# Kernel tuning notes

Measured on AMD Instinct MI355X. Metric: run time of the kernel, lower is better.

Reference implementation:

```python
import jax, jax.numpy as jnp
import numpy as np

N, E = 50000, 800000
HID, HEADS, EDIM = 64, 4, 3
NEG_SLOPE = 0.2
LN_EPS = 1e-5


def setup_inputs() -> dict:
    key = jax.random.key(0)
    ks = jax.random.split(key, 12)
    h = jax.random.normal(ks[0], (N, HID), dtype=jnp.float32)
    edge_index = jax.random.randint(ks[1], (2, E), 0, N, dtype=jnp.int64)
    edge_attr = jax.random.normal(ks[2], (E, EDIM), dtype=jnp.float32)
    t = jax.random.uniform(ks[3], (1,), dtype=jnp.float32)
    s = 1.0 / np.sqrt(HID)
    W = jax.random.normal(ks[4], (HID, HEADS * HID), dtype=jnp.float32) * s
    att_src = jax.random.normal(ks[5], (1, HEADS, HID), dtype=jnp.float32) * s
    att_dst = jax.random.normal(ks[6], (1, HEADS, HID), dtype=jnp.float32) * s
    W_edge = jax.random.normal(ks[7], (EDIM, HEADS * HID), dtype=jnp.float32) * s
    att_edge = jax.random.normal(ks[8], (1, HEADS, HID), dtype=jnp.float32) * s
    bias = jnp.zeros((HID,), dtype=jnp.float32)
    ln_gamma = jnp.ones((HID,), dtype=jnp.float32)
    ln_beta = jnp.zeros((HID,), dtype=jnp.float32)
    return {"t": t, "h": h, "edge_index": edge_index, "edge_attr": edge_attr,
            "W": W, "att_src": att_src, "att_dst": att_dst, "W_edge": W_edge,
            "att_edge": att_edge, "bias": bias, "ln_gamma": ln_gamma, "ln_beta": ln_beta}


def reference(t, h, edge_index, edge_attr, W, att_src, att_dst, W_edge, att_edge, bias, ln_gamma, ln_beta):
    # GATConv (PyG, edge_dim>0, add_self_loops=False, concat=False, eval mode)
    x = (h @ W).reshape(N, HEADS, HID)                     # [N,H,C]
    a_src = (x * att_src).sum(-1)                          # [N,H]
    a_dst = (x * att_dst).sum(-1)                          # [N,H]
    e = (edge_attr @ W_edge).reshape(E, HEADS, HID)        # [E,H,C]
    a_edge = (e * att_edge).sum(-1)                        # [E,H]
    src, dst = edge_index[0], edge_index[1]
    alpha = a_src[src] + a_dst[dst] + a_edge               # [E,H]
    alpha = jax.nn.leaky_relu(alpha, NEG_SLOPE)
    # softmax over edges sharing the same destination node
    amax = jax.ops.segment_max(alpha, dst, num_segments=N)  # [N,H]
    ex = jnp.exp(alpha - amax[dst])
    esum = jax.ops.segment_sum(ex, dst, num_segments=N)     # [N,H]
    alpha = ex / (esum[dst] + 1e-16)
    msg = x[src] * alpha[:, :, None]                        # [E,H,C]
    out = jax.ops.segment_sum(msg, dst, num_segments=N)     # [N,H,C]
    out = out.mean(axis=1) + bias                           # concat=False -> head mean
    # LayerNorm + SiLU
    mu = out.mean(-1, keepdims=True)
    var = ((out - mu) ** 2).mean(-1, keepdims=True)
    y = (out - mu) * jax.lax.rsqrt(var + LN_EPS) * ln_gamma + ln_beta
    return y * jax.nn.sigmoid(y)
```

## Files before the change

kernel.cpp:

```cpp
#include <hip/hip_runtime.h>
#include <hip/hip_bf16.h>

#define HIDC 64
#define NEG_SLOPE 0.2f
#define SCAN_G 128

typedef __hip_bfloat16 bf16;
typedef short bf16x8 __attribute__((ext_vector_type(8)));
typedef float floatx4 __attribute__((ext_vector_type(4)));

static __device__ __forceinline__ float b2f(bf16 v) { return __bfloat162float(v); }

static __device__ __forceinline__ unsigned short f2us(float f) {
  bf16 b = __float2bfloat16(f);
  union { bf16 b; unsigned short u; } c;
  c.b = b;
  return c.u;
}

template <bool FF>
static __device__ __forceinline__ float ld(const void* __restrict__ p, size_t i) {
  return FF ? ((const float*)p)[i] : b2f(((const bf16*)p)[i]);
}
static __device__ __forceinline__ float ldr(const void* __restrict__ p, size_t i,
                                            bool ff) {
  return ff ? ((const float*)p)[i] : b2f(((const bf16*)p)[i]);
}
template <bool I64>
static __device__ __forceinline__ int ldi(const int* __restrict__ p, long long i) {
  return I64 ? (int)((const long long*)p)[i] : p[i];
}
static __device__ __forceinline__ int clampN(int v, int N) {
  return ((unsigned)v < (unsigned)N) ? v : 0;
}

static __device__ __forceinline__ bool det_f32(const unsigned* __restrict__ hw) {
  unsigned w = hw[threadIdx.x & 31];
  int ex = (w >> 7) & 0xFF;
  unsigned long long b = __ballot(ex >= 99 && ex <= 135);
  return __popcll(b) < 32;
}
static __device__ __forceinline__ bool det_i64(const int* __restrict__ ei) {
  int v = ei[2 * (threadIdx.x & 31) + 1];
  return __ballot(v != 0) == 0ULL;
}

template <bool FF, bool I64>
static __device__ __forceinline__ void xh_body(
    const void* __restrict__ h, const void* __restrict__ W,
    const void* __restrict__ att_src, const void* __restrict__ att_dst,
    const int* __restrict__ ei, bf16* __restrict__ x,
    float* __restrict__ a_src, float* __restrict__ a_dst,
    int* __restrict__ cnt, int N, int E,
    unsigned short* __restrict__ hls, unsigned short* __restrict__ wls) {
  for (long long e = (long long)blockIdx.x * 256 + threadIdx.x; e < E;
       e += (long long)gridDim.x * 256) {
    int dst = clampN(ldi<I64>(ei, (long long)E + e), N);
    atomicAdd(&cnt[dst], 1);
  }
  const int t = threadIdx.x;
  const long long n0 = (long long)blockIdx.x * 64;
  {
    const int c = t;
#pragma unroll
    for (int q = 0; q < 8; q++) {
      unsigned short u[8];
#pragma unroll
      for (int j = 0; j < 8; j++) {
        int k = q * 8 + j;
        u[j] = FF ? f2us(((const float*)W)[(size_t)k * 256 + c])
                  : ((const unsigned short*)W)[(size_t)k * 256 + c];
      }
      int4 v = make_int4((int)(u[0] | ((unsigned)u[1] << 16)),
                         (int)(u[2] | ((unsigned)u[3] << 16)),
                         (int)(u[4] | ((unsigned)u[5] << 16)),
                         (int)(u[6] | ((unsigned)u[7] << 16)));
      *(int4*)&wls[c * 64 + (q ^ (c & 7)) * 8] = v;
    }
  }
  {
    const int row = t >> 2;
    const long long n = n0 + row;
#pragma unroll
    for (int dq = 0; dq < 2; dq++) {
      int q = (t & 3) * 2 + dq;
      int4 v;
      if (n < N) {
        if (FF) {
          const float4* hp = (const float4*)h + n * 16 + q * 2;
          float4 f0 = hp[0], f1 = hp[1];
          v = make_int4((int)(f2us(f0.x) | ((unsigned)f2us(f0.y) << 16)),
                        (int)(f2us(f0.z) | ((unsigned)f2us(f0.w) << 16)),
                        (int)(f2us(f1.x) | ((unsigned)f2us(f1.y) << 16)),
                        (int)(f2us(f1.z) | ((unsigned)f2us(f1.w) << 16)));
        } else {
          v = *((const int4*)((const unsigned short*)h + n * 64 + q * 8));
        }
      } else {
        v = make_int4(0, 0, 0, 0);
      }
      *(int4*)&hls[row * 64 + (q ^ (row & 7)) * 8] = v;
    }
  }
  __syncthreads();
  const int w = t >> 6;
  const int lane = t & 63;
  const int lm = lane & 15, lq = lane >> 4;
  bf16x8 af[4][2];
#pragma unroll
  for (int nt = 0; nt < 4; nt++)
#pragma unroll
    for (int ks = 0; ks < 2; ks++) {
      int m = nt * 16 + lm;
      int q = ks * 4 + lq;
      af[nt][ks] = *(const bf16x8*)&hls[m * 64 + (q ^ (m & 7)) * 8];
    }
  floatx4 acc[4][4];
#pragma unroll
  for (int nt = 0; nt < 4; nt++)
#pragma unroll
    for (int ct = 0; ct < 4; ct++) acc[nt][ct] = (floatx4){0.f, 0.f, 0.f, 0.f};
#pragma unroll
  for (int ct = 0; ct < 4; ct++) {
    int c = w * 64 + ct * 16 + lm;
    bf16x8 b0 = *(const bf16x8*)&wls[c * 64 + ((lq) ^ (c & 7)) * 8];
    bf16x8 b1 = *(const bf16x8*)&wls[c * 64 + ((4 + lq) ^ (c & 7)) * 8];
#pragma unroll
    for (int nt = 0; nt < 4; nt++) {
      acc[nt][ct] = __builtin_amdgcn_mfma_f32_16x16x32_bf16(af[nt][0], b0,
                                                            acc[nt][ct], 0, 0, 0);
      acc[nt][ct] = __builtin_amdgcn_mfma_f32_16x16x32_bf16(af[nt][1], b1,
                                                            acc[nt][ct], 0, 0, 0);
    }
  }
  float as_c[4], ad_c[4];
#pragma unroll
  for (int ct = 0; ct < 4; ct++) {
    as_c[ct] = ld<FF>(att_src, w * 64 + ct * 16 + lm);
    ad_c[ct] = ld<FF>(att_dst, w * 64 + ct * 16 + lm);
  }
#pragma unroll
  for (int nt = 0; nt < 4; nt++) {
    float ps[4] = {0.f, 0.f, 0.f, 0.f}, pd[4] = {0.f, 0.f, 0.f, 0.f};
#pragma unroll
    for (int ct = 0; ct < 4; ct++) {
#pragma unroll
      for (int r = 0; r < 4; r++) {
        ps[r] += acc[nt][ct][r] * as_c[ct];
        pd[r] += acc[nt][ct][r] * ad_c[ct];
      }
    }
    long long nb = n0 + nt * 16 + lq * 4;
#pragma unroll
    for (int r = 0; r < 4; r++) {
      long long n = nb + r;
      if (n < N) {
#pragma unroll
        for (int ct = 0; ct < 4; ct++)
          x[n * 256 + w * 64 + ct * 16 + lm] = __float2bfloat16(acc[nt][ct][r]);
      }
    }
#pragma unroll
    for (int mask = 1; mask < 16; mask <<= 1) {
#pragma unroll
      for (int r = 0; r < 4; r++) {
        ps[r] += __shfl_xor(ps[r], mask);
        pd[r] += __shfl_xor(pd[r], mask);
      }
    }
    if (lm == 0) {
#pragma unroll
      for (int r = 0; r < 4; r++) {
        long long n = nb + r;
        if (n < N) {
          a_src[n * 4 + w] = ps[r];
          a_dst[n * 4 + w] = pd[r];
        }
      }
    }
  }
}

__global__ void __launch_bounds__(256) k_xh(
    const void* __restrict__ h, const void* __restrict__ W,
    const void* __restrict__ att_src, const void* __restrict__ att_dst,
    const int* __restrict__ ei, bf16* __restrict__ x,
    float* __restrict__ a_src, float* __restrict__ a_dst,
    int* __restrict__ cnt, int N, int E) {
  __shared__ alignas(16) unsigned short hls[64 * 64];
  __shared__ alignas(16) unsigned short wls[256 * 64];
  bool f32 = det_f32((const unsigned*)h);
  bool i64 = det_i64(ei);
  if (f32) {
    if (i64) xh_body<true, true>(h, W, att_src, att_dst, ei, x, a_src, a_dst, cnt, N, E, hls, wls);
    else     xh_body<true, false>(h, W, att_src, att_dst, ei, x, a_src, a_dst, cnt, N, E, hls, wls);
  } else {
    if (i64) xh_body<false, true>(h, W, att_src, att_dst, ei, x, a_src, a_dst, cnt, N, E, hls, wls);
    else     xh_body<false, false>(h, W, att_src, att_dst, ei, x, a_src, a_dst, cnt, N, E, hls, wls);
  }
}

__global__ void __launch_bounds__(1024) k_bscan(
    const void* __restrict__ W_edge, const void* __restrict__ att_edge,
    const unsigned* __restrict__ hw, const int* __restrict__ cnt,
    int* __restrict__ offs, int* __restrict__ bsum, int* __restrict__ bbase,
    int* __restrict__ done, float* __restrict__ M, int N) {
  int b = blockIdx.x, t = threadIdx.x;
  if (b == 0 && t < 768) {
    bool ff = det_f32(hw);
    int wv = t >> 6, lane = t & 63;
    int d = wv >> 2, hh = wv & 3;
    float p = ldr(W_edge, (size_t)d * 256 + hh * 64 + lane, ff) *
              ldr(att_edge, (size_t)hh * 64 + lane, ff);
#pragma unroll
    for (int o = 32; o; o >>= 1) p += __shfl_down(p, o);
    if (lane == 0) M[d * 4 + hh] = p;
  }
  const int C = (N + SCAN_G - 1) / SCAN_G;
  const int b0 = b * C;
  __shared__ int ts[1024];
  __shared__ int lastf;
  int v = 0;
  if (t < C && b0 + t < N) v = cnt[b0 + t];
  ts[t] = v;
  __syncthreads();
  for (int off = 1; off < 1024; off <<= 1) {
    int u = (t >= off) ? ts[t - off] : 0;
    __syncthreads();
    ts[t] += u;
    __syncthreads();
  }
  if (t < C && b0 + t < N) offs[b0 + t] = ts[t] - v;
  if (t == 1023) {
    atomicExch(&bsum[b], ts[1023]);
    __threadfence();
    int old = atomicAdd(done, 1);
    lastf = (old == SCAN_G - 1) ? 1 : 0;
  }
  __syncthreads();
  if (lastf) {
    int w = (t < SCAN_G) ? atomicAdd(&bsum[t], 0) : 0;
    ts[t] = w;
    __syncthreads();
    for (int off = 1; off < 1024; off <<= 1) {
      int u = (t >= off) ? ts[t - off] : 0;
      __syncthreads();
      ts[t] += u;
      __syncthreads();
    }
    if (t < SCAN_G) bbase[t] = ts[t] - w;
  }
}

__global__ void __launch_bounds__(1024) k_add(
    int* __restrict__ offs, int* __restrict__ cursor,
    const int* __restrict__ bbase, int N, int E) {
  int b = blockIdx.x, t = threadIdx.x;
  const int C = (N + SCAN_G - 1) / SCAN_G;
  const int b0 = b * C;
  int base = bbase[b];
  if (t < C && b0 + t < N) {
    int o = offs[b0 + t] + base;
    offs[b0 + t] = o;
    cursor[b0 + t] = o;
  }
  if (b == 0 && t == 0) offs[N] = E;
}

template <bool FF, bool I64>
static __device__ __forceinline__ void es_body(
    const int* __restrict__ ei, const void* __restrict__ eattr,
    const float* __restrict__ a_src, const float* __restrict__ a_dst,
    const float* __restrict__ M, int* __restrict__ cursor,
    int4* __restrict__ slots, int E, int N, unsigned* __restrict__ sattr) {
  const long long e0 = (long long)blockIdx.x * 256;
  {
    const unsigned bpe = FF ? 12u : 6u;
    const unsigned* gsrc = (const unsigned*)((const char*)eattr + e0 * bpe);
    unsigned ndw = FF ? 768u : 384u;
    long long bytes_left = ((long long)E - e0) * bpe;
    if (bytes_left < 0) bytes_left = 0;
    unsigned max_dw = (unsigned)((bytes_left + 3) >> 2);
    if (ndw > max_dw) ndw = max_dw;
    for (unsigned i = threadIdx.x; i < ndw; i += 256) sattr[i] = gsrc[i];
  }
  __syncthreads();
  long long e = e0 + threadIdx.x;
  if (e >= E) return;
  int src = clampN(ldi<I64>(ei, e), N);
  int dst = clampN(ldi<I64>(ei, (long long)E + e), N);
  float ea0, ea1, ea2;
  if (FF) {
    const float* sf = (const float*)sattr;
    ea0 = sf[threadIdx.x * 3 + 0];
    ea1 = sf[threadIdx.x * 3 + 1];
    ea2 = sf[threadIdx.x * 3 + 2];
  } else {
    const unsigned short* su = (const unsigned short*)sattr;
    ea0 = __uint_as_float((unsigned)su[threadIdx.x * 3 + 0] << 16);
    ea1 = __uint_as_float((unsigned)su[threadIdx.x * 3 + 1] << 16);
    ea2 = __uint_as_float((unsigned)su[threadIdx.x * 3 + 2] << 16);
  }
  const float4 m0 = ((const float4*)M)[0];
  const float4 m1 = ((const float4*)M)[1];
  const float4 m2 = ((const float4*)M)[2];
  const float4 as4 = ((const float4*)a_src)[src];
  const float4 ad4 = ((const float4*)a_dst)[dst];
  float al[4];
  al[0] = as4.x + ad4.x + ea0 * m0.x + ea1 * m1.x + ea2 * m2.x;
  al[1] = as4.y + ad4.y + ea0 * m0.y + ea1 * m1.y + ea2 * m2.y;
  al[2] = as4.z + ad4.z + ea0 * m0.z + ea1 * m1.z + ea2 * m2.z;
  al[3] = as4.w + ad4.w + ea0 * m0.w + ea1 * m1.w + ea2 * m2.w;
  unsigned short u[4];
#pragma unroll
  for (int hh = 0; hh < 4; hh++) {
    float a = al[hh];
    a = (a > 0.f) ? a : NEG_SLOPE * a;
    a = fminf(fmaxf(a, -60.f), 60.f);
    u[hh] = f2us(__expf(a));
  }
  int pos = atomicAdd(&cursor[dst], 1);
  slots[pos] = make_int4(src, (int)(u[0] | ((unsigned)u[1] << 16)),
                         (int)(u[2] | ((unsigned)u[3] << 16)), 0);
}

__global__ void __launch_bounds__(256) k_es(
    const int* __restrict__ ei, const void* __restrict__ eattr,
    const float* __restrict__ a_src, const float* __restrict__ a_dst,
    const float* __restrict__ M, const unsigned* __restrict__ hw,
    int* __restrict__ cursor, int4* __restrict__ slots, int E, int N) {
  __shared__ unsigned sattr[768];
  bool f32 = det_f32(hw);
  bool i64 = det_i64(ei);
  if (f32) {
    if (i64) es_body<true, true>(ei, eattr, a_src, a_dst, M, cursor, slots, E, N, sattr);
    else     es_body<true, false>(ei, eattr, a_src, a_dst, M, cursor, slots, E, N, sattr);
  } else {
    if (i64) es_body<false, true>(ei, eattr, a_src, a_dst, M, cursor, slots, E, N, sattr);
    else     es_body<false, false>(ei, eattr, a_src, a_dst, M, cursor, slots, E, N, sattr);
  }
}

template <bool HZ>
static __device__ __forceinline__ void agg_loop(
    const int4* __restrict__ slots, const unsigned* __restrict__ xw,
    int s0, int s1, bool hi_half, float& a0o, float& a1o, float& wso) {
  float a0 = 0.f, a1 = 0.f, ws = 0.f;
  int i = s0;
  for (; i + 4 <= s1; i += 4) {
    int4 q0 = slots[i], q1 = slots[i + 1], q2 = slots[i + 2], q3 = slots[i + 3];
    unsigned d0 = xw[(size_t)((unsigned)q0.x << 7)];
    unsigned d1 = xw[(size_t)((unsigned)q1.x << 7)];
    unsigned d2 = xw[(size_t)((unsigned)q2.x << 7)];
    unsigned d3 = xw[(size_t)((unsigned)q3.x << 7)];
    unsigned p0 = HZ ? (unsigned)q0.z : (unsigned)q0.y;
    unsigned p1 = HZ ? (unsigned)q1.z : (unsigned)q1.y;
    unsigned p2 = HZ ? (unsigned)q2.z : (unsigned)q2.y;
    unsigned p3 = HZ ? (unsigned)q3.z : (unsigned)q3.y;
    float w0 = __uint_as_float(hi_half ? (p0 & 0xffff0000u) : (p0 << 16));
    float w1 = __uint_as_float(hi_half ? (p1 & 0xffff0000u) : (p1 << 16));
    float w2 = __uint_as_float(hi_half ? (p2 & 0xffff0000u) : (p2 << 16));
    float w3 = __uint_as_float(hi_half ? (p3 & 0xffff0000u) : (p3 << 16));
    a0 += w0 * __uint_as_float(d0 << 16);
    a1 += w0 * __uint_as_float(d0 & 0xffff0000u);
    a0 += w1 * __uint_as_float(d1 << 16);
    a1 += w1 * __uint_as_float(d1 & 0xffff0000u);
    a0 += w2 * __uint_as_float(d2 << 16);
    a1 += w2 * __uint_as_float(d2 & 0xffff0000u);
    a0 += w3 * __uint_as_float(d3 << 16);
    a1 += w3 * __uint_as_float(d3 & 0xffff0000u);
    ws += (w0 + w1) + (w2 + w3);
  }
  for (; i < s1; i++) {
    int4 q = slots[i];
    unsigned d = xw[(size_t)((unsigned)q.x << 7)];
    unsigned pz = HZ ? (unsigned)q.z : (unsigned)q.y;
    float wv = __uint_as_float(hi_half ? (pz & 0xffff0000u) : (pz << 16));
    a0 += wv * __uint_as_float(d << 16);
    a1 += wv * __uint_as_float(d & 0xffff0000u);
    ws += wv;
  }
  a0o = a0; a1o = a1; wso = ws;
}

__global__ void __launch_bounds__(256) k_agg(
    const int* __restrict__ offs, const int4* __restrict__ slots,
    const unsigned* __restrict__ xu, const unsigned* __restrict__ hw,
    const void* __restrict__ bias, const void* __restrict__ gamma,
    const void* __restrict__ beta, void* __restrict__ out, int N) {
  __shared__ float sh[2][256];
  int t = threadIdx.x;
  int w = t >> 6, lane = t & 63;
  int nl = w >> 1;
  int hb2 = w & 1;
  int n = blockIdx.x * 2 + nl;
  if (n < N) {
    const unsigned* xw = xu + hb2 * 64 + lane;
    int s0 = offs[n], s1 = offs[n + 1];
    bool hi_half = lane >= 32;
    float a0, a1, ws;
    if (hb2) agg_loop<true>(slots, xw, s0, s1, hi_half, a0, a1, ws);
    else     agg_loop<false>(slots, xw, s0, s1, hi_half, a0, a1, ws);
    float inv = 1.f / (ws + 1e-16f);
    int head = hb2 * 2 + (hi_half ? 1 : 0);
    int pidx = lane & 31;
    sh[nl][head * 64 + 2 * pidx] = a0 * inv;
    sh[nl][head * 64 + 2 * pidx + 1] = a1 * inv;
  }
  __syncthreads();
  if ((t & 127) < 64) {
    int nl2 = t >> 7;
    int n2 = blockIdx.x * 2 + nl2;
    if (n2 < N) {
      int c = t & 63;
      bool ff = det_f32(hw);
      float m = (sh[nl2][c] + sh[nl2][64 + c] + sh[nl2][128 + c] +
                 sh[nl2][192 + c]) * 0.25f + ldr(bias, c, ff);
      float mu = m;
#pragma unroll
      for (int off = 32; off; off >>= 1) mu += __shfl_xor(mu, off);
      mu *= (1.f / 64.f);
      float d = m - mu;
      float v = d * d;
#pragma unroll
      for (int off = 32; off; off >>= 1) v += __shfl_xor(v, off);
      v *= (1.f / 64.f);
      float y = d * rsqrtf(v + 1e-5f) * ldr(gamma, c, ff) + ldr(beta, c, ff);
      float sig = 1.f / (1.f + __expf(-y));
      float r = y * sig;
      size_t oi = (size_t)n2 * 64 + c;
      if (ff) ((float*)out)[oi] = r;
      else ((bf16*)out)[oi] = __float2bfloat16(r);
    }
  }
}

extern "C" void kernel_launch(void* const* d_in, const int* in_sizes, int n_in,
                              void* d_out, int out_size, void* d_ws,
                              size_t ws_size, hipStream_t stream) {
  const void* h        = d_in[1];
  const int*  ei       = (const int*)d_in[2];
  const void* eattr    = d_in[3];
  const void* W        = d_in[4];
  const void* att_src  = d_in[5];
  const void* att_dst  = d_in[6];
  const void* W_edge   = d_in[7];
  const void* att_edge = d_in[8];
  const void* bias     = d_in[9];
  const void* gamma    = d_in[10];
  const void* beta     = d_in[11];

  const int N = in_sizes[1] / HIDC;
  const int E = in_sizes[3] / 3;

  char* p = (char*)d_ws;
  float* M    = (float*)p; p += 64;
  bf16* x     = (bf16*)p;  p += (size_t)N * 256 * 2;
  float* asrc = (float*)p; p += (size_t)N * 4 * 4;
  float* adst = (float*)p; p += (size_t)N * 4 * 4;
  int4* slots = (int4*)p;  p += (size_t)E * 16;
  int* cnt    = (int*)p;   p += (size_t)N * 4;
  int* done   = (int*)p;   p += 64;
  int* offs   = (int*)p;   p += ((size_t)N + 4) * 4;
  int* cursor = (int*)p;   p += (size_t)N * 4;
  int* bsum   = (int*)p;   p += SCAN_G * 4;
  int* bbase  = (int*)p;   p += SCAN_G * 4;

  size_t need = (size_t)(p - (char*)d_ws);
  if (ws_size < need || N <= 0 || E <= 0) {
    hipMemsetAsync(d_out, 0, (size_t)out_size * 2, stream);
    return;
  }

  hipMemsetAsync(cnt, 0, (size_t)N * 4 + 64, stream);

  k_xh<<<(N + 63) / 64, 256, 0, stream>>>(h, W, att_src, att_dst, ei, x,
                                          asrc, adst, cnt, N, E);
  k_bscan<<<SCAN_G, 1024, 0, stream>>>(W_edge, att_edge, (const unsigned*)h,
                                       cnt, offs, bsum, bbase, done, M, N);
  k_add<<<SCAN_G, 1024, 0, stream>>>(offs, cursor, bbase, N, E);
  k_es<<<(E + 255) / 256, 256, 0, stream>>>(ei, eattr, asrc, adst, M,
                                            (const unsigned*)h, cursor, slots,
                                            E, N);
  k_agg<<<(N + 1) / 2, 256, 0, stream>>>(offs, slots, (const unsigned*)x,
                                         (const unsigned*)h, bias, gamma, beta,
                                         d_out, N);
}
```

Measured before the change: 277.9 us.

## Use one wave per node in aggregation, wave-shuffle scan, two edges per thread

The aggregation kernel now gives each destination node one 64-lane wave. Each lane loads 4 bf16 features via uint2 and does the head-mean and LayerNorm with shuffles instead of shared memory. The block scan replaces its shared-memory Hillis-Steele loop, with two barriers per step, by wave-level shuffle scans. The edge-score kernel handles 512 edges per block with two edges per thread and hoists the M loads. The aim is fewer barriers, less per-edge slot re-reading across waves, and wider gathers, at the cost of less parallelism per high-degree node.

Result: slower. 288.0 us (+3.6%).

```diff
diff --git a/kernel.cpp b/kernel.cpp
--- a/kernel.cpp
+++ b/kernel.cpp
@@ -43,6 +43,15 @@
 static __device__ __forceinline__ bool det_i64(const int* __restrict__ ei) {
   int v = ei[2 * (threadIdx.x & 31) + 1];
   return __ballot(v != 0) == 0ULL;
+}
+
+static __device__ __forceinline__ int wave_iscan(int v, int lane) {
+#pragma unroll
+  for (int off = 1; off < 64; off <<= 1) {
+    int u = __shfl_up(v, off);
+    if (lane >= off) v += u;
+  }
+  return v;
 }
 
 template <bool FF, bool I64>
@@ -206,10 +215,10 @@
     int* __restrict__ offs, int* __restrict__ bsum, int* __restrict__ bbase,
     int* __restrict__ done, float* __restrict__ M, int N) {
   int b = blockIdx.x, t = threadIdx.x;
+  int lane = t & 63, wvi = t >> 6;
   if (b == 0 && t < 768) {
     bool ff = det_f32(hw);
-    int wv = t >> 6, lane = t & 63;
-    int d = wv >> 2, hh = wv & 3;
+    int d = wvi >> 2, hh = wvi & 3;
     float p = ldr(W_edge, (size_t)d * 256 + hh * 64 + lane, ff) *
               ldr(att_edge, (size_t)hh * 64 + lane, ff);
 #pragma unroll
@@ -218,37 +227,42 @@
   }
   const int C = (N + SCAN_G - 1) / SCAN_G;
   const int b0 = b * C;
-  __shared__ int ts[1024];
+  __shared__ int wsum[16];
   __shared__ int lastf;
-  int v = 0;
-  if (t < C && b0 + t < N) v = cnt[b0 + t];
-  ts[t] = v;
+  int v = (t < C && b0 + t < N) ? cnt[b0 + t] : 0;
+  int inc = wave_iscan(v, lane);
+  if (lane == 63) wsum[wvi] = inc;
   __syncthreads();
-  for (int off = 1; off < 1024; off <<= 1) {
-    int u = (t >= off) ? ts[t - off] : 0;
-    __syncthreads();
-    ts[t] += u;
-    __syncthreads();
-  }
-  if (t < C && b0 + t < N) offs[b0 + t] = ts[t] - v;
-  if (t == 1023) {
-    atomicExch(&bsum[b], ts[1023]);
+  if (wvi == 0) {
+    int sv = (lane < 16) ? wsum[lane] : 0;
+    sv = wave_iscan(sv, lane);
+    if (lane < 16) wsum[lane] = sv;
+  }
+  __syncthreads();
+  int base = wvi ? wsum[wvi - 1] : 0;
+  int total = wsum[15];
+  if (t < C && b0 + t < N) offs[b0 + t] = inc + base - v;
+  if (t == 0) {
+    atomicExch(&bsum[b], total);
     __threadfence();
     int old = atomicAdd(done, 1);
     lastf = (old == SCAN_G - 1) ? 1 : 0;
   }
   __syncthreads();
   if (lastf) {
-    int w = (t < SCAN_G) ? atomicAdd(&bsum[t], 0) : 0;
-    ts[t] = w;
+    int v2 = (t < SCAN_G) ? atomicAdd(&bsum[t], 0) : 0;
+    int inc2 = wave_iscan(v2, lane);
     __syncthreads();
-    for (int off = 1; off < 1024; off <<= 1) {
-      int u = (t >= off) ? ts[t - off] : 0;
-      __syncthreads();
-      ts[t] += u;
-      __syncthreads();
-    }
-    if (t < SCAN_G) bbase[t] = ts[t] - w;
+    if (lane == 63) wsum[wvi] = inc2;
+    __syncthreads();
+    if (wvi == 0) {
+      int sv = (lane < 16) ? wsum[lane] : 0;
+      sv = wave_iscan(sv, lane);
+      if (lane < 16) wsum[lane] = sv;
+    }
+    __syncthreads();
+    int base2 = wvi ? wsum[wvi - 1] : 0;
+    if (t < SCAN_G) bbase[t] = inc2 + base2 - v2;
   }
 }
 
@@ -268,42 +282,27 @@
 }
 
 template <bool FF, bool I64>
-static __device__ __forceinline__ void es_body(
-    const int* __restrict__ ei, const void* __restrict__ eattr,
-    const float* __restrict__ a_src, const float* __restrict__ a_dst,
-    const float* __restrict__ M, int* __restrict__ cursor,
-    int4* __restrict__ slots, int E, int N, unsigned* __restrict__ sattr) {
-  const long long e0 = (long long)blockIdx.x * 256;
-  {
-    const unsigned bpe = FF ? 12u : 6u;
-    const unsigned* gsrc = (const unsigned*)((const char*)eattr + e0 * bpe);
-    unsigned ndw = FF ? 768u : 384u;
-    long long bytes_left = ((long long)E - e0) * bpe;
-    if (bytes_left < 0) bytes_left = 0;
-    unsigned max_dw = (unsigned)((bytes_left + 3) >> 2);
-    if (ndw > max_dw) ndw = max_dw;
-    for (unsigned i = threadIdx.x; i < ndw; i += 256) sattr[i] = gsrc[i];
-  }
-  __syncthreads();
-  long long e = e0 + threadIdx.x;
+static __device__ __forceinline__ void es_one(
+    const int* __restrict__ ei, const unsigned* __restrict__ sattr, int j,
+    long long e, const float* __restrict__ a_src,
+    const float* __restrict__ a_dst, const float4 m0, const float4 m1,
+    const float4 m2, int* __restrict__ cursor, int4* __restrict__ slots,
+    int E, int N) {
   if (e >= E) return;
   int src = clampN(ldi<I64>(ei, e), N);
   int dst = clampN(ldi<I64>(ei, (long long)E + e), N);
   float ea0, ea1, ea2;
   if (FF) {
     const float* sf = (const float*)sattr;
-    ea0 = sf[threadIdx.x * 3 + 0];
-    ea1 = sf[threadIdx.x * 3 + 1];
-    ea2 = sf[threadIdx.x * 3 + 2];
+    ea0 = sf[j * 3 + 0];
+    ea1 = sf[j * 3 + 1];
+    ea2 = sf[j * 3 + 2];
   } else {
     const unsigned short* su = (const unsigned short*)sattr;
-    ea0 = __uint_as_float((unsigned)su[threadIdx.x * 3 + 0] << 16);
-    ea1 = __uint_as_float((unsigned)su[threadIdx.x * 3 + 1] << 16);
-    ea2 = __uint_as_float((unsigned)su[threadIdx.x * 3 + 2] << 16);
-  }
-  const float4 m0 = ((const float4*)M)[0];
-  const float4 m1 = ((const float4*)M)[1];
-  const float4 m2 = ((const float4*)M)[2];
+    ea0 = __uint_as_float((unsigned)su[j * 3 + 0] << 16);
+    ea1 = __uint_as_float((unsigned)su[j * 3 + 1] << 16);
+    ea2 = __uint_as_float((unsigned)su[j * 3 + 2] << 16);
+  }
   const float4 as4 = ((const float4*)a_src)[src];
   const float4 ad4 = ((const float4*)a_dst)[dst];
   float al[4];
@@ -324,12 +323,40 @@
                          (int)(u[2] | ((unsigned)u[3] << 16)), 0);
 }
 
+template <bool FF, bool I64>
+static __device__ __forceinline__ void es_body(
+    const int* __restrict__ ei, const void* __restrict__ eattr,
+    const float* __restrict__ a_src, const float* __restrict__ a_dst,
+    const float* __restrict__ M, int* __restrict__ cursor,
+    int4* __restrict__ slots, int E, int N, unsigned* __restrict__ sattr) {
+  const long long e0 = (long long)blockIdx.x * 512;
+  {
+    const unsigned bpe = FF ? 12u : 6u;
+    const unsigned* gsrc = (const unsigned*)((const char*)eattr + e0 * bpe);
+    unsigned ndw = FF ? 1536u : 768u;
+    long long bytes_left = ((long long)E - e0) * bpe;
+    if (bytes_left < 0) bytes_left = 0;
+    unsigned max_dw = (unsigned)((bytes_left + 3) >> 2);
+    if (ndw > max_dw) ndw = max_dw;
+    for (unsigned i = threadIdx.x; i < ndw; i += 256) sattr[i] = gsrc[i];
+  }
+  __syncthreads();
+  const float4 m0 = ((const float4*)M)[0];
+  const float4 m1 = ((const float4*)M)[1];
+  const float4 m2 = ((const float4*)M)[2];
+  int t = threadIdx.x;
+  es_one<FF, I64>(ei, sattr, t, e0 + t, a_src, a_dst, m0, m1, m2, cursor,
+                  slots, E, N);
+  es_one<FF, I64>(ei, sattr, t + 256, e0 + t + 256, a_src, a_dst, m0, m1, m2,
+                  cursor, slots, E, N);
+}
+
 __global__ void __launch_bounds__(256) k_es(
     const int* __restrict__ ei, const void* __restrict__ eattr,
     const float* __restrict__ a_src, const float* __restrict__ a_dst,
     const float* __restrict__ M, const unsigned* __restrict__ hw,
     int* __restrict__ cursor, int4* __restrict__ slots, int E, int N) {
-  __shared__ unsigned sattr[768];
+  __shared__ unsigned sattr[1536];
   bool f32 = det_f32(hw);
   bool i64 = det_i64(ei);
   if (f32) {
@@ -341,96 +368,102 @@
   }
 }
 
-template <bool HZ>
-static __device__ __forceinline__ void agg_loop(
-    const int4* __restrict__ slots, const unsigned* __restrict__ xw,
-    int s0, int s1, bool hi_half, float& a0o, float& a1o, float& wso) {
-  float a0 = 0.f, a1 = 0.f, ws = 0.f;
+__global__ void __launch_bounds__(256) k_agg(
+    const int* __restrict__ offs, const int4* __restrict__ slots,
+    const uint2* __restrict__ xr, const unsigned* __restrict__ hw,
+    const void* __restrict__ bias, const void* __restrict__ gamma,
+    const void* __restrict__ beta, void* __restrict__ out, int N) {
+  const int t = threadIdx.x;
+  const int wv = t >> 6, lane = t & 63;
+  const bool ff = det_f32(hw);
+  const int n = blockIdx.x * 4 + wv;
+  if (n >= N) return;
+  const int h = lane >> 4;
+  const int sh_w = (h & 1) ? 0 : 16;
+  const bool hz = (h & 2) != 0;
+  int s0 = offs[n], s1 = offs[n + 1];
+  float a0 = 0.f, a1 = 0.f, a2 = 0.f, a3 = 0.f, ws = 0.f;
   int i = s0;
   for (; i + 4 <= s1; i += 4) {
     int4 q0 = slots[i], q1 = slots[i + 1], q2 = slots[i + 2], q3 = slots[i + 3];
-    unsigned d0 = xw[(size_t)((unsigned)q0.x << 7)];
-    unsigned d1 = xw[(size_t)((unsigned)q1.x << 7)];
-    unsigned d2 = xw[(size_t)((unsigned)q2.x << 7)];
-    unsigned d3 = xw[(size_t)((unsigned)q3.x << 7)];
-    unsigned p0 = HZ ? (unsigned)q0.z : (unsigned)q0.y;
-    unsigned p1 = HZ ? (unsigned)q1.z : (unsigned)q1.y;
-    unsigned p2 = HZ ? (unsigned)q2.z : (unsigned)q2.y;
-    unsigned p3 = HZ ? (unsigned)q3.z : (unsigned)q3.y;
-    float w0 = __uint_as_float(hi_half ? (p0 & 0xffff0000u) : (p0 << 16));
-    float w1 = __uint_as_float(hi_half ? (p1 & 0xffff0000u) : (p1 << 16));
-    float w2 = __uint_as_float(hi_half ? (p2 & 0xffff0000u) : (p2 << 16));
-    float w3 = __uint_as_float(hi_half ? (p3 & 0xffff0000u) : (p3 << 16));
-    a0 += w0 * __uint_as_float(d0 << 16);
-    a1 += w0 * __uint_as_float(d0 & 0xffff0000u);
-    a0 += w1 * __uint_as_float(d1 << 16);
-    a1 += w1 * __uint_as_float(d1 & 0xffff0000u);
-    a0 += w2 * __uint_as_float(d2 << 16);
-    a1 += w2 * __uint_as_float(d2 & 0xffff0000u);
-    a0 += w3 * __uint_as_float(d3 << 16);
-    a1 += w3 * __uint_as_float(d3 & 0xffff0000u);
+    uint2 d0 = xr[(size_t)(unsigned)q0.x * 64 + lane];
+    uint2 d1 = xr[(size_t)(unsigned)q1.x * 64 + lane];
+    uint2 d2 = xr[(size_t)(unsigned)q2.x * 64 + lane];
+    uint2 d3 = xr[(size_t)(unsigned)q3.x * 64 + lane];
+    unsigned p0 = hz ? (unsigned)q0.z : (unsigned)q0.y;
+    unsigned p1 = hz ? (unsigned)q1.z : (unsigned)q1.y;
+    unsigned p2 = hz ? (unsigned)q2.z : (unsigned)q2.y;
+    unsigned p3 = hz ? (unsigned)q3.z : (unsigned)q3.y;
+    float w0 = __uint_as_float((p0 << sh_w) & 0xffff0000u);
+    float w1 = __uint_as_float((p1 << sh_w) & 0xffff0000u);
+    float w2 = __uint_as_float((p2 << sh_w) & 0xffff0000u);
+    float w3 = __uint_as_float((p3 << sh_w) & 0xffff0000u);
+    a0 += w0 * __uint_as_float(d0.x << 16);
+    a1 += w0 * __uint_as_float(d0.x & 0xffff0000u);
+    a2 += w0 * __uint_as_float(d0.y << 16);
+    a3 += w0 * __uint_as_float(d0.y & 0xffff0000u);
+    a0 += w1 * __uint_as_float(d1.x << 16);
+    a1 += w1 * __uint_as_float(d1.x & 0xffff0000u);
+    a2 += w1 * __uint_as_float(d1.y << 16);
+    a3 += w1 * __uint_as_float(d1.y & 0xffff0000u);
+    a0 += w2 * __uint_as_float(d2.x << 16);
+    a1 += w2 * __uint_as_float(d2.x & 0xffff0000u);
+    a2 += w2 * __uint_as_float(d2.y << 16);
+    a3 += w2 * __uint_as_float(d2.y & 0xffff0000u);
+    a0 += w3 * __uint_as_float(d3.x << 16);
+    a1 += w3 * __uint_as_float(d3.x & 0xffff0000u);
+    a2 += w3 * __uint_as_float(d3.y << 16);
+    a3 += w3 * __uint_as_float(d3.y & 0xffff0000u);
     ws += (w0 + w1) + (w2 + w3);
   }
   for (; i < s1; i++) {
     int4 q = slots[i];
-    unsigned d = xw[(size_t)((unsigned)q.x << 7)];
-    unsigned pz = HZ ? (unsigned)q.z : (unsigned)q.y;
-    float wv = __uint_as_float(hi_half ? (pz & 0xffff0000u) : (pz << 16));
-    a0 += wv * __uint_as_float(d << 16);
-    a1 += wv * __uint_as_float(d & 0xffff0000u);
-    ws += wv;
-  }
-  a0o = a0; a1o = a1; wso = ws;
-}
-
-__global__ void __launch_bounds__(256) k_agg(
-    const int* __restrict__ offs, const int4* __restrict__ slots,
-    const unsigned* __restrict__ xu, const unsigned* __restrict__ hw,
-    const void* __restrict__ bias, const void* __restrict__ gamma,
-    const void* __restrict__ beta, void* __restrict__ out, int N) {
-  __shared__ float sh[2][256];
-  int t = threadIdx.x;
-  int w = t >> 6, lane = t & 63;
-  int nl = w >> 1;
-  int hb2 = w & 1;
-  int n = blockIdx.x * 2 + nl;
-  if (n < N) {
-    const unsigned* xw = xu + hb2 * 64 + lane;
-    int s0 = offs[n], s1 = offs[n + 1];
-    bool hi_half = lane >= 32;
-    float a0, a1, ws;
-    if (hb2) agg_loop<true>(slots, xw, s0, s1, hi_half, a0, a1, ws);
-    else     agg_loop<false>(slots, xw, s0, s1, hi_half, a0, a1, ws);
-    float inv = 1.f / (ws + 1e-16f);
-    int head = hb2 * 2 + (hi_half ? 1 : 0);
-    int pidx = lane & 31;
-    sh[nl][head * 64 + 2 * pidx] = a0 * inv;
-    sh[nl][head * 64 + 2 * pidx + 1] = a1 * inv;
-  }
-  __syncthreads();
-  if ((t & 127) < 64) {
-    int nl2 = t >> 7;
-    int n2 = blockIdx.x * 2 + nl2;
-    if (n2 < N) {
-      int c = t & 63;
-      bool ff = det_f32(hw);
-      float m = (sh[nl2][c] + sh[nl2][64 + c] + sh[nl2][128 + c] +
-                 sh[nl2][192 + c]) * 0.25f + ldr(bias, c, ff);
-      float mu = m;
-#pragma unroll
-      for (int off = 32; off; off >>= 1) mu += __shfl_xor(mu, off);
-      mu *= (1.f / 64.f);
-      float d = m - mu;
-      float v = d * d;
-#pragma unroll
-      for (int off = 32; off; off >>= 1) v += __shfl_xor(v, off);
-      v *= (1.f / 64.f);
-      float y = d * rsqrtf(v + 1e-5f) * ldr(gamma, c, ff) + ldr(beta, c, ff);
-      float sig = 1.f / (1.f + __expf(-y));
-      float r = y * sig;
-      size_t oi = (size_t)n2 * 64 + c;
-      if (ff) ((float*)out)[oi] = r;
-      else ((bf16*)out)[oi] = __float2bfloat16(r);
+    uint2 d = xr[(size_t)(unsigned)q.x * 64 + lane];
+    unsigned p = hz ? (unsigned)q.z : (unsigned)q.y;
+    float w = __uint_as_float((p << sh_w) & 0xffff0000u);
+    a0 += w * __uint_as_float(d.x << 16);
+    a1 += w * __uint_as_float(d.x & 0xffff0000u);
+    a2 += w * __uint_as_float(d.y << 16);
+    a3 += w * __uint_as_float(d.y & 0xffff0000u);
+    ws += w;
+  }
+  float inv = 1.f / (ws + 1e-16f);
+  float m0 = a0 * inv, m1 = a1 * inv, m2 = a2 * inv, m3 = a3 * inv;
+  m0 += __shfl_xor(m0, 16); m0 += __shfl_xor(m0, 32);
+  m1 += __shfl_xor(m1, 16); m1 += __shfl_xor(m1, 32);
+  m2 += __shfl_xor(m2, 16); m2 += __shfl_xor(m2, 32);
+  m3 += __shfl_xor(m3, 16); m3 += __shfl_xor(m3, 32);
+  const int cb = (lane & 15) * 4;
+  m0 = m0 * 0.25f + ldr(bias, cb + 0, ff);
+  m1 = m1 * 0.25f + ldr(bias, cb + 1, ff);
+  m2 = m2 * 0.25f + ldr(bias, cb + 2, ff);
+  m3 = m3 * 0.25f + ldr(bias, cb + 3, ff);
+  float s = (m0 + m1) + (m2 + m3);
+#pragma unroll
+  for (int mask = 1; mask < 16; mask <<= 1) s += __shfl_xor(s, mask);
+  float mu = s * (1.f / 64.f);
+  float d0 = m0 - mu, d1 = m1 - mu, d2 = m2 - mu, d3 = m3 - mu;
+  float v = (d0 * d0 + d1 * d1) + (d2 * d2 + d3 * d3);
+#pragma unroll
+  for (int mask = 1; mask < 16; mask <<= 1) v += __shfl_xor(v, mask);
+  float rs = rsqrtf(v * (1.f / 64.f) + 1e-5f);
+  float y0 = d0 * rs * ldr(gamma, cb + 0, ff) + ldr(beta, cb + 0, ff);
+  float y1 = d1 * rs * ldr(gamma, cb + 1, ff) + ldr(beta, cb + 1, ff);
+  float y2 = d2 * rs * ldr(gamma, cb + 2, ff) + ldr(beta, cb + 2, ff);
+  float y3 = d3 * rs * ldr(gamma, cb + 3, ff) + ldr(beta, cb + 3, ff);
+  float r0 = y0 / (1.f + __expf(-y0));
+  float r1 = y1 / (1.f + __expf(-y1));
+  float r2 = y2 / (1.f + __expf(-y2));
+  float r3 = y3 / (1.f + __expf(-y3));
+  if (lane < 16) {
+    if (ff) {
+      float4 o = make_float4(r0, r1, r2, r3);
+      ((float4*)out)[(size_t)n * 16 + lane] = o;
+    } else {
+      uint2 o;
+      o.x = (unsigned)f2us(r0) | ((unsigned)f2us(r1) << 16);
+      o.y = (unsigned)f2us(r2) | ((unsigned)f2us(r3) << 16);
+      ((uint2*)out)[(size_t)n * 16 + lane] = o;
     }
   }
 }
@@ -479,10 +512,10 @@
   k_bscan<<<SCAN_G, 1024, 0, stream>>>(W_edge, att_edge, (const unsigned*)h,
                                        cnt, offs, bsum, bbase, done, M, N);
   k_add<<<SCAN_G, 1024, 0, stream>>>(offs, cursor, bbase, N, E);
-  k_es<<<(E + 255) / 256, 256, 0, stream>>>(ei, eattr, asrc, adst, M,
+  k_es<<<(E + 511) / 512, 256, 0, stream>>>(ei, eattr, asrc, adst, M,
                                             (const unsigned*)h, cursor, slots,
                                             E, N);
-  k_agg<<<(N + 1) / 2, 256, 0, stream>>>(offs, slots, (const unsigned*)x,
+  k_agg<<<(N + 3) / 4, 256, 0, stream>>>(offs, slots, (const uint2*)x,
                                          (const unsigned*)h, bias, gamma, beta,
                                          d_out, N);
 }
```

## Use wave-shuffle scan, nontemporal slot traffic, deeper agg unroll, split agg launch

Applied to the files above, without the earlier changes.

Replaces the LDS Hillis-Steele block scan with a two-level wave shuffle scan to cut barriers. The edge scatter kernel processes two edges per thread and writes slots with nontemporal stores. The aggregation loop is unrolled to 8 edges with nontemporal slot loads for more gathers in flight. Aggregation is split into two launches over node halves. Nontemporal hints may reduce cache reuse, since the slots are read by two waves per node, and the extra launch adds overhead.

Result: slower. 322.4 us (+16.0%).

```diff
diff --git a/kernel.cpp b/kernel.cpp
--- a/kernel.cpp
+++ b/kernel.cpp
@@ -8,6 +8,7 @@
 typedef __hip_bfloat16 bf16;
 typedef short bf16x8 __attribute__((ext_vector_type(8)));
 typedef float floatx4 __attribute__((ext_vector_type(4)));
+typedef int intx4 __attribute__((ext_vector_type(4)));
 
 static __device__ __forceinline__ float b2f(bf16 v) { return __bfloat162float(v); }
 
@@ -43,6 +44,15 @@
 static __device__ __forceinline__ bool det_i64(const int* __restrict__ ei) {
   int v = ei[2 * (threadIdx.x & 31) + 1];
   return __ballot(v != 0) == 0ULL;
+}
+
+static __device__ __forceinline__ int wave_iscan(int v, int lane) {
+#pragma unroll
+  for (int off = 1; off < 64; off <<= 1) {
+    int u = __shfl_up(v, off);
+    if (lane >= off) v += u;
+  }
+  return v;
 }
 
 template <bool FF, bool I64>
@@ -206,10 +216,10 @@
     int* __restrict__ offs, int* __restrict__ bsum, int* __restrict__ bbase,
     int* __restrict__ done, float* __restrict__ M, int N) {
   int b = blockIdx.x, t = threadIdx.x;
+  int lane = t & 63, wvi = t >> 6;
   if (b == 0 && t < 768) {
     bool ff = det_f32(hw);
-    int wv = t >> 6, lane = t & 63;
-    int d = wv >> 2, hh = wv & 3;
+    int d = wvi >> 2, hh = wvi & 3;
     float p = ldr(W_edge, (size_t)d * 256 + hh * 64 + lane, ff) *
               ldr(att_edge, (size_t)hh * 64 + lane, ff);
 #pragma unroll
@@ -218,37 +228,42 @@
   }
   const int C = (N + SCAN_G - 1) / SCAN_G;
   const int b0 = b * C;
-  __shared__ int ts[1024];
+  __shared__ int wsum[16];
   __shared__ int lastf;
-  int v = 0;
-  if (t < C && b0 + t < N) v = cnt[b0 + t];
-  ts[t] = v;
+  int v = (t < C && b0 + t < N) ? cnt[b0 + t] : 0;
+  int inc = wave_iscan(v, lane);
+  if (lane == 63) wsum[wvi] = inc;
   __syncthreads();
-  for (int off = 1; off < 1024; off <<= 1) {
-    int u = (t >= off) ? ts[t - off] : 0;
-    __syncthreads();
-    ts[t] += u;
-    __syncthreads();
-  }
-  if (t < C && b0 + t < N) offs[b0 + t] = ts[t] - v;
-  if (t == 1023) {
-    atomicExch(&bsum[b], ts[1023]);
+  if (wvi == 0) {
+    int sv = (lane < 16) ? wsum[lane] : 0;
+    sv = wave_iscan(sv, lane);
+    if (lane < 16) wsum[lane] = sv;
+  }
+  __syncthreads();
+  int base = wvi ? wsum[wvi - 1] : 0;
+  int total = wsum[15];
+  if (t < C && b0 + t < N) offs[b0 + t] = inc + base - v;
+  if (t == 0) {
+    atomicExch(&bsum[b], total);
     __threadfence();
     int old = atomicAdd(done, 1);
     lastf = (old == SCAN_G - 1) ? 1 : 0;
   }
   __syncthreads();
   if (lastf) {
-    int w = (t < SCAN_G) ? atomicAdd(&bsum[t], 0) : 0;
-    ts[t] = w;
+    int v2 = (t < SCAN_G) ? atomicAdd(&bsum[t], 0) : 0;
+    int inc2 = wave_iscan(v2, lane);
     __syncthreads();
-    for (int off = 1; off < 1024; off <<= 1) {
-      int u = (t >= off) ? ts[t - off] : 0;
-      __syncthreads();
-      ts[t] += u;
-      __syncthreads();
-    }
-    if (t < SCAN_G) bbase[t] = ts[t] - w;
+    if (lane == 63) wsum[wvi] = inc2;
+    __syncthreads();
+    if (wvi == 0) {
+      int sv = (lane < 16) ? wsum[lane] : 0;
+      sv = wave_iscan(sv, lane);
+      if (lane < 16) wsum[lane] = sv;
+    }
+    __syncthreads();
+    int base2 = wvi ? wsum[wvi - 1] : 0;
+    if (t < SCAN_G) bbase[t] = inc2 + base2 - v2;
   }
 }
 
@@ -268,42 +283,27 @@
 }
 
 template <bool FF, bool I64>
-static __device__ __forceinline__ void es_body(
-    const int* __restrict__ ei, const void* __restrict__ eattr,
-    const float* __restrict__ a_src, const float* __restrict__ a_dst,
-    const float* __restrict__ M, int* __restrict__ cursor,
-    int4* __restrict__ slots, int E, int N, unsigned* __restrict__ sattr) {
-  const long long e0 = (long long)blockIdx.x * 256;
-  {
-    const unsigned bpe = FF ? 12u : 6u;
-    const unsigned* gsrc = (const unsigned*)((const char*)eattr + e0 * bpe);
-    unsigned ndw = FF ? 768u : 384u;
-    long long bytes_left = ((long long)E - e0) * bpe;
-    if (bytes_left < 0) bytes_left = 0;
-    unsigned max_dw = (unsigned)((bytes_left + 3) >> 2);
-    if (ndw > max_dw) ndw = max_dw;
-    for (unsigned i = threadIdx.x; i < ndw; i += 256) sattr[i] = gsrc[i];
-  }
-  __syncthreads();
-  long long e = e0 + threadIdx.x;
+static __device__ __forceinline__ void es_one(
+    const int* __restrict__ ei, const unsigned* __restrict__ sattr, int j,
+    long long e, const float* __restrict__ a_src,
+    const float* __restrict__ a_dst, const float4 m0, const float4 m1,
+    const float4 m2, int* __restrict__ cursor, intx4* __restrict__ slots,
+    int E, int N) {
   if (e >= E) return;
   int src = clampN(ldi<I64>(ei, e), N);
   int dst = clampN(ldi<I64>(ei, (long long)E + e), N);
   float ea0, ea1, ea2;
   if (FF) {
     const float* sf = (const float*)sattr;
-    ea0 = sf[threadIdx.x * 3 + 0];
-    ea1 = sf[threadIdx.x * 3 + 1];
-    ea2 = sf[threadIdx.x * 3 + 2];
+    ea0 = sf[j * 3 + 0];
+    ea1 = sf[j * 3 + 1];
+    ea2 = sf[j * 3 + 2];
   } else {
     const unsigned short* su = (const unsigned short*)sattr;
-    ea0 = __uint_as_float((unsigned)su[threadIdx.x * 3 + 0] << 16);
-    ea1 = __uint_as_float((unsigned)su[threadIdx.x * 3 + 1] << 16);
-    ea2 = __uint_as_float((unsigned)su[threadIdx.x * 3 + 2] << 16);
-  }
-  const float4 m0 = ((const float4*)M)[0];
-  const float4 m1 = ((const float4*)M)[1];
-  const float4 m2 = ((const float4*)M)[2];
+    ea0 = __uint_as_float((unsigned)su[j * 3 + 0] << 16);
+    ea1 = __uint_as_float((unsigned)su[j * 3 + 1] << 16);
+    ea2 = __uint_as_float((unsigned)su[j * 3 + 2] << 16);
+  }
   const float4 as4 = ((const float4*)a_src)[src];
   const float4 ad4 = ((const float4*)a_dst)[dst];
   float al[4];
@@ -320,16 +320,45 @@
     u[hh] = f2us(__expf(a));
   }
   int pos = atomicAdd(&cursor[dst], 1);
-  slots[pos] = make_int4(src, (int)(u[0] | ((unsigned)u[1] << 16)),
-                         (int)(u[2] | ((unsigned)u[3] << 16)), 0);
+  intx4 v = {src, (int)(u[0] | ((unsigned)u[1] << 16)),
+             (int)(u[2] | ((unsigned)u[3] << 16)), 0};
+  __builtin_nontemporal_store(v, &slots[pos]);
+}
+
+template <bool FF, bool I64>
+static __device__ __forceinline__ void es_body(
+    const int* __restrict__ ei, const void* __restrict__ eattr,
+    const float* __restrict__ a_src, const float* __restrict__ a_dst,
+    const float* __restrict__ M, int* __restrict__ cursor,
+    intx4* __restrict__ slots, int E, int N, unsigned* __restrict__ sattr) {
+  const long long e0 = (long long)blockIdx.x * 512;
+  {
+    const unsigned bpe = FF ? 12u : 6u;
+    const unsigned* gsrc = (const unsigned*)((const char*)eattr + e0 * bpe);
+    unsigned ndw = FF ? 1536u : 768u;
+    long long bytes_left = ((long long)E - e0) * bpe;
+    if (bytes_left < 0) bytes_left = 0;
+    unsigned max_dw = (unsigned)((bytes_left + 3) >> 2);
+    if (ndw > max_dw) ndw = max_dw;
+    for (unsigned i = threadIdx.x; i < ndw; i += 256) sattr[i] = gsrc[i];
+  }
+  __syncthreads();
+  const float4 m0 = ((const float4*)M)[0];
+  const float4 m1 = ((const float4*)M)[1];
+  const float4 m2 = ((const float4*)M)[2];
+  int t = threadIdx.x;
+  es_one<FF, I64>(ei, sattr, t, e0 + t, a_src, a_dst, m0, m1, m2, cursor,
+                  slots, E, N);
+  es_one<FF, I64>(ei, sattr, t + 256, e0 + t + 256, a_src, a_dst, m0, m1, m2,
+                  cursor, slots, E, N);
 }
 
 __global__ void __launch_bounds__(256) k_es(
     const int* __restrict__ ei, const void* __restrict__ eattr,
     const float* __restrict__ a_src, const float* __restrict__ a_dst,
     const float* __restrict__ M, const unsigned* __restrict__ hw,
-    int* __restrict__ cursor, int4* __restrict__ slots, int E, int N) {
-  __shared__ unsigned sattr[768];
+    int* __restrict__ cursor, intx4* __restrict__ slots, int E, int N) {
+  __shared__ unsigned sattr[1536];
   bool f32 = det_f32(hw);
   bool i64 = det_i64(ei);
   if (f32) {
@@ -343,36 +372,29 @@
 
 template <bool HZ>
 static __device__ __forceinline__ void agg_loop(
-    const int4* __restrict__ slots, const unsigned* __restrict__ xw,
+    const intx4* __restrict__ slots, const unsigned* __restrict__ xw,
     int s0, int s1, bool hi_half, float& a0o, float& a1o, float& wso) {
   float a0 = 0.f, a1 = 0.f, ws = 0.f;
   int i = s0;
-  for (; i + 4 <= s1; i += 4) {
-    int4 q0 = slots[i], q1 = slots[i + 1], q2 = slots[i + 2], q3 = slots[i + 3];
-    unsigned d0 = xw[(size_t)((unsigned)q0.x << 7)];
-    unsigned d1 = xw[(size_t)((unsigned)q1.x << 7)];
-    unsigned d2 = xw[(size_t)((unsigned)q2.x << 7)];
-    unsigned d3 = xw[(size_t)((unsigned)q3.x << 7)];
-    unsigned p0 = HZ ? (unsigned)q0.z : (unsigned)q0.y;
-    unsigned p1 = HZ ? (unsigned)q1.z : (unsigned)q1.y;
-    unsigned p2 = HZ ? (unsigned)q2.z : (unsigned)q2.y;
-    unsigned p3 = HZ ? (unsigned)q3.z : (unsigned)q3.y;
-    float w0 = __uint_as_float(hi_half ? (p0 & 0xffff0000u) : (p0 << 16));
-    float w1 = __uint_as_float(hi_half ? (p1 & 0xffff0000u) : (p1 << 16));
-    float w2 = __uint_as_float(hi_half ? (p2 & 0xffff0000u) : (p2 << 16));
-    float w3 = __uint_as_float(hi_half ? (p3 & 0xffff0000u) : (p3 << 16));
-    a0 += w0 * __uint_as_float(d0 << 16);
-    a1 += w0 * __uint_as_float(d0 & 0xffff0000u);
-    a0 += w1 * __uint_as_float(d1 << 16);
-    a1 += w1 * __uint_as_float(d1 & 0xffff0000u);
-    a0 += w2 * __uint_as_float(d2 << 16);
-    a1 += w2 * __uint_as_float(d2 & 0xffff0000u);
-    a0 += w3 * __uint_as_float(d3 << 16);
-    a1 += w3 * __uint_as_float(d3 & 0xffff0000u);
-    ws += (w0 + w1) + (w2 + w3);
+  for (; i + 8 <= s1; i += 8) {
+    intx4 q[8];
+#pragma unroll
+    for (int j = 0; j < 8; j++) q[j] = __builtin_nontemporal_load(&slots[i + j]);
+    unsigned d[8];
+#pragma unroll
+    for (int j = 0; j < 8; j++)
+      d[j] = xw[(size_t)((unsigned)q[j].x << 7)];
+#pragma unroll
+    for (int j = 0; j < 8; j++) {
+      unsigned p = HZ ? (unsigned)q[j].z : (unsigned)q[j].y;
+      float w = __uint_as_float(hi_half ? (p & 0xffff0000u) : (p << 16));
+      a0 += w * __uint_as_float(d[j] << 16);
+      a1 += w * __uint_as_float(d[j] & 0xffff0000u);
+      ws += w;
+    }
   }
   for (; i < s1; i++) {
-    int4 q = slots[i];
+    intx4 q = __builtin_nontemporal_load(&slots[i]);
     unsigned d = xw[(size_t)((unsigned)q.x << 7)];
     unsigned pz = HZ ? (unsigned)q.z : (unsigned)q.y;
     float wv = __uint_as_float(hi_half ? (pz & 0xffff0000u) : (pz << 16));
@@ -384,17 +406,18 @@
 }
 
 __global__ void __launch_bounds__(256) k_agg(
-    const int* __restrict__ offs, const int4* __restrict__ slots,
+    const int* __restrict__ offs, const intx4* __restrict__ slots,
     const unsigned* __restrict__ xu, const unsigned* __restrict__ hw,
     const void* __restrict__ bias, const void* __restrict__ gamma,
-    const void* __restrict__ beta, void* __restrict__ out, int N) {
+    const void* __restrict__ beta, void* __restrict__ out, int nbase,
+    int nend) {
   __shared__ float sh[2][256];
   int t = threadIdx.x;
   int w = t >> 6, lane = t & 63;
   int nl = w >> 1;
   int hb2 = w & 1;
-  int n = blockIdx.x * 2 + nl;
-  if (n < N) {
+  int n = nbase + blockIdx.x * 2 + nl;
+  if (n < nend) {
     const unsigned* xw = xu + hb2 * 64 + lane;
     int s0 = offs[n], s1 = offs[n + 1];
     bool hi_half = lane >= 32;
@@ -410,8 +433,8 @@
   __syncthreads();
   if ((t & 127) < 64) {
     int nl2 = t >> 7;
-    int n2 = blockIdx.x * 2 + nl2;
-    if (n2 < N) {
+    int n2 = nbase + blockIdx.x * 2 + nl2;
+    if (n2 < nend) {
       int c = t & 63;
       bool ff = det_f32(hw);
       float m = (sh[nl2][c] + sh[nl2][64 + c] + sh[nl2][128 + c] +
@@ -458,7 +481,7 @@
   bf16* x     = (bf16*)p;  p += (size_t)N * 256 * 2;
   float* asrc = (float*)p; p += (size_t)N * 4 * 4;
   float* adst = (float*)p; p += (size_t)N * 4 * 4;
-  int4* slots = (int4*)p;  p += (size_t)E * 16;
+  intx4* slots= (intx4*)p; p += (size_t)E * 16;
   int* cnt    = (int*)p;   p += (size_t)N * 4;
   int* done   = (int*)p;   p += 64;
   int* offs   = (int*)p;   p += ((size_t)N + 4) * 4;
@@ -479,10 +502,17 @@
   k_bscan<<<SCAN_G, 1024, 0, stream>>>(W_edge, att_edge, (const unsigned*)h,
                                        cnt, offs, bsum, bbase, done, M, N);
   k_add<<<SCAN_G, 1024, 0, stream>>>(offs, cursor, bbase, N, E);
-  k_es<<<(E + 255) / 256, 256, 0, stream>>>(ei, eattr, asrc, adst, M,
+  k_es<<<(E + 511) / 512, 256, 0, stream>>>(ei, eattr, asrc, adst, M,
                                             (const unsigned*)h, cursor, slots,
                                             E, N);
-  k_agg<<<(N + 1) / 2, 256, 0, stream>>>(offs, slots, (const unsigned*)x,
-                                         (const unsigned*)h, bias, gamma, beta,
-                                         d_out, N);
-}
+  int N1 = ((N / 2) + 1) & ~1;
+  if (N1 > N) N1 = N;
+  k_agg<<<(N1 + 1) / 2, 256, 0, stream>>>(offs, slots, (const unsigned*)x,
+                                          (const unsigned*)h, bias, gamma,
+                                          beta, d_out, 0, N1);
+  if (N > N1)
+    k_agg<<<(N - N1 + 1) / 2, 256, 0, stream>>>(offs, slots,
+                                                (const unsigned*)x,
+                                                (const unsigned*)h, bias,
+                                                gamma, beta, d_out, N1, N);
+}
```
